# Performance work log

Hardware: AMD Instinct MI355X
Metric: run time of the kernel (lower is better)

Reference implementation:

```python
import jax, jax.numpy as jnp
import numpy as np

INPUT_SIZE = 1024
HIDDEN_SIZE = 1024
B, L = 32, 2048


def setup_inputs() -> dict:
    key = jax.random.key(0)
    k_h, k_m, k_lw, k_vw, k_vq = jax.random.split(key, 5)
    h = jax.random.normal(k_h, (B, L, INPUT_SIZE), dtype=jnp.float32)
    mask = jax.random.randint(k_m, (B, L), 0, 2).astype(bool)
    # nn.Linear(input+hidden, hidden): weight (hidden, input+hidden), bias (hidden,)
    fan = INPUT_SIZE + HIDDEN_SIZE + HIDDEN_SIZE
    ln_w = jax.random.uniform(k_lw, (HIDDEN_SIZE, INPUT_SIZE + HIDDEN_SIZE),
                              minval=-1.0, maxval=1.0, dtype=jnp.float32) * np.sqrt(6.0 / fan)
    ln_b = jnp.zeros((HIDDEN_SIZE,), dtype=jnp.float32)
    # v: Linear(hidden, 1, bias=False) -> weight (1, hidden); store as (hidden,)
    v_w = jax.random.uniform(k_vw, (HIDDEN_SIZE,), minval=-1.0, maxval=1.0,
                             dtype=jnp.float32) * np.sqrt(6.0 / (HIDDEN_SIZE + 1))
    vq = jax.random.uniform(k_vq, (HIDDEN_SIZE,), dtype=jnp.float32)
    return {"h": h, "mask": mask, "ln_w": ln_w, "ln_b": ln_b, "v_w": v_w, "vq": vq}


def reference(h, mask, ln_w, ln_b, v_w, vq):
    # ln(cat([h, vq], -1)) == h @ W_h^T + vq @ W_vq^T + b  (vq is constant over b,l)
    W_h = ln_w[:, :INPUT_SIZE]          # (H, I)
    W_vq = ln_w[:, INPUT_SIZE:]         # (H, H)
    bias = ln_b + W_vq @ vq             # (H,)
    pre = jnp.einsum('bli,hi->blh', h, W_h) + bias  # (B, L, H)
    s = jnp.tanh(pre) @ v_w             # (B, L)
    s = s - (~mask).astype(s.dtype) * 10000.0
    a = jax.nn.softmax(s, axis=1)       # softmax over seq dim
    r = jnp.einsum('bl,bli->bi', a, h)  # (B, I)
    return r  # dropout omitted (eval mode)
```

## Files before the change

kernel.cpp:

```cpp
#include <hip/hip_runtime.h>
#include <hip/hip_bf16.h>

typedef short  bf16x8s __attribute__((ext_vector_type(8)));
typedef float  f32x4   __attribute__((ext_vector_type(4)));

#define BATCH 32
#define SEQL  2048
#define NROWS (BATCH * SEQL)
#define IN    1024
#define HID   1024

#define WHB_OFF   0u
#define BIAS_OFF  0x200000u
#define SPART_OFF 0x210000u
#define ABUF_OFF  0x610000u
#define HB_OFF    0x650000u
#define WS_NEED_BF16 ((size_t)HB_OFF + (size_t)NROWS * IN * 2)

__device__ __forceinline__ unsigned int pack2bf(float f0, float f1) {
    unsigned int u0 = __float_as_uint(f0) + 0x8000u;
    unsigned int u1 = __float_as_uint(f1) + 0x8000u;
    return __builtin_amdgcn_perm(u1, u0, 0x07060302u);
}

__device__ __forceinline__ float tanh_fast(float x) {
    float xc = fminf(fmaxf(x, -15.f), 15.f);
    float t  = __builtin_amdgcn_exp2f(xc * 2.8853900817779268f);
    return (t - 1.f) * __builtin_amdgcn_rcpf(t + 1.f);
}

__device__ __forceinline__ void gl2lds16(const void* g, void* l) {
    __builtin_amdgcn_global_load_lds(
        (const __attribute__((address_space(1))) unsigned int*)g,
        (__attribute__((address_space(3))) unsigned int*)l, 16, 0, 0);
}

__device__ __forceinline__ void block_map(int bi, int& rb, int& cb) {
    int xcd  = bi & 7;
    int slot = bi >> 3;
    rb = xcd + 8 * (slot >> 3);
    cb = slot & 7;
}

__global__ __launch_bounds__(256) void prep_kernel(const float* __restrict__ ln_w,
                                                   const float* __restrict__ ln_b,
                                                   const float* __restrict__ vq,
                                                   const float* __restrict__ h,
                                                   unsigned short* __restrict__ whb,
                                                   float* __restrict__ bias,
                                                   unsigned short* __restrict__ hb) {
    const int bi = blockIdx.x;
    const int t  = threadIdx.x;
    if (bi < 1024) {
        const int n = bi;
        const int wave = t >> 6;
        const int lane = t & 63;
        float4 v = ((const float4*)(ln_w + (size_t)n * 2048))[t];
        uint2 pk;
        pk.x = pack2bf(v.x, v.y);
        pk.y = pack2bf(v.z, v.w);
        *(uint2*)(whb + (size_t)n * 1024 + t * 4) = pk;
        const float* wrow = ln_w + (size_t)n * 2048 + 1024;
        float s = 0.f;
        #pragma unroll
        for (int j = 0; j < 4; ++j) {
            int k = t + j * 256;
            s += wrow[k] * vq[k];
        }
        #pragma unroll
        for (int off = 32; off; off >>= 1) s += __shfl_xor(s, off);
        __shared__ float red[4];
        if (lane == 0) red[wave] = s;
        __syncthreads();
        if (t == 0) bias[n] = ln_b[n] + red[0] + red[1] + red[2] + red[3];
    } else {
        size_t idx = ((size_t)(bi - 1024) * 256 + t) * 8;
        float4 a = *(const float4*)(h + idx);
        float4 b = *(const float4*)(h + idx + 4);
        uint4 p;
        p.x = pack2bf(a.x, a.y); p.y = pack2bf(a.z, a.w);
        p.z = pack2bf(b.x, b.y); p.w = pack2bf(b.z, b.w);
        *(uint4*)(hb + idx) = p;
    }
}

__global__ __launch_bounds__(512) void gemm256_kernel(const unsigned short* __restrict__ hb,
                                                      const unsigned short* __restrict__ whb,
                                                      const float* __restrict__ bias,
                                                      const float* __restrict__ vw,
                                                      float* __restrict__ s_part) {
    __shared__ __align__(16) unsigned short As[8192];
    __shared__ __align__(16) unsigned short Bs[4096];

    const int tid = threadIdx.x;
    int rb, cb;
    block_map(blockIdx.x, rb, cb);
    const int wave = tid >> 6;
    const int lane = tid & 63;
    const int quad = lane >> 4;
    const int l15  = lane & 15;
    const int wy   = wave >> 1;
    const int wx   = wave & 1;
    const int row0 = rb * 256;
    const int col0 = cb * 128;

    const int srow = tid >> 2;
    const int sg   = tid & 3;
    const int swz  = (srow >> 1) & 3;
    const unsigned short* gA0 = hb  + (size_t)(row0 + srow) * 1024 + ((sg ^ swz) * 8);
    const unsigned short* gA1 = gA0 + (size_t)128 * 1024;
    const unsigned short* gB0 = whb + (size_t)(col0 + srow) * 1024 + ((sg ^ swz) * 8);
    unsigned short* lA0 = As + tid * 8;
    unsigned short* lA1 = As + 4096 + tid * 8;
    unsigned short* lB0 = Bs + tid * 8;

    const unsigned short* rA[4];
    const unsigned short* rB[4];
    #pragma unroll
    for (int i = 0; i < 4; ++i) {
        int ra = wy * 64 + i * 16 + l15;
        rA[i] = As + ra * 32 + ((quad ^ ((ra >> 1) & 3)) * 8);
        int rn = wx * 64 + i * 16 + l15;
        rB[i] = Bs + rn * 32 + ((quad ^ ((rn >> 1) & 3)) * 8);
    }

    f32x4 acc[4][4];
    #pragma unroll
    for (int i = 0; i < 4; ++i)
        #pragma unroll
        for (int j = 0; j < 4; ++j)
            acc[i][j] = (f32x4){0.f, 0.f, 0.f, 0.f};

    for (int k0 = 0; k0 < 1024; k0 += 32) {
        __syncthreads();
        gl2lds16(gA0 + k0, lA0);
        gl2lds16(gA1 + k0, lA1);
        gl2lds16(gB0 + k0, lB0);
        __syncthreads();

        bf16x8s af[4], bfv[4];
        #pragma unroll
        for (int i = 0; i < 4; ++i) af[i]  = *(const bf16x8s*)rA[i];
        #pragma unroll
        for (int i = 0; i < 4; ++i) bfv[i] = *(const bf16x8s*)rB[i];
        #pragma unroll
        for (int mt = 0; mt < 4; ++mt)
            #pragma unroll
            for (int nt = 0; nt < 4; ++nt)
                acc[mt][nt] = __builtin_amdgcn_mfma_f32_16x16x32_bf16(af[mt], bfv[nt], acc[mt][nt], 0, 0, 0);
    }

    const int colb = col0 + wx * 64 + l15;
    float vwv[4], bv[4];
    #pragma unroll
    for (int nt = 0; nt < 4; ++nt) {
        vwv[nt] = vw[colb + nt * 16];
        bv[nt]  = bias[colb + nt * 16];
    }
    const int rowb = row0 + wy * 64 + quad * 4;
    float* sp = s_part + (size_t)(cb * 2 + wx) * NROWS;
    #pragma unroll
    for (int mt = 0; mt < 4; ++mt) {
        #pragma unroll
        for (int r = 0; r < 4; ++r) {
            float p = 0.f;
            #pragma unroll
            for (int nt = 0; nt < 4; ++nt)
                p += tanh_fast(acc[mt][nt][r] + bv[nt]) * vwv[nt];
            p += __shfl_xor(p, 1);
            p += __shfl_xor(p, 2);
            p += __shfl_xor(p, 4);
            p += __shfl_xor(p, 8);
            if (l15 == 0) sp[rowb + mt * 16 + r] = p;
        }
    }
}

__global__ __launch_bounds__(256) void gemm_f32_kernel(const float* __restrict__ hmat,
                                                       const unsigned short* __restrict__ whb,
                                                       const float* __restrict__ bias,
                                                       const float* __restrict__ vw,
                                                       float* __restrict__ s_part) {
    __shared__ __align__(16) unsigned short As[4096];
    __shared__ __align__(16) unsigned short Bs[4096];
    const int tid = threadIdx.x;
    int rb, cb;
    block_map(blockIdx.x, rb, cb);
    const int wave = tid >> 6;
    const int lane = tid & 63;
    const int quad = lane >> 4;
    const int l15  = lane & 15;
    const int wy   = wave >> 1;
    const int wx   = wave & 1;
    const int row0 = rb * 128;
    const int col0 = cb * 128;
    const int srow = tid >> 2;
    const int sg   = tid & 3;
    const int swz  = (srow >> 1) & 3;
    const float*          gA0 = hmat + (size_t)(row0 + srow)      * 1024 + sg * 8;
    const float*          gA1 = hmat + (size_t)(row0 + srow + 64) * 1024 + sg * 8;
    const unsigned short* gB0 = whb  + (size_t)(col0 + srow)      * 1024 + ((sg ^ swz) * 8);
    unsigned short* wA0 = As + srow * 32 + ((sg ^ swz) * 8);
    unsigned short* wA1 = wA0 + 64 * 32;
    unsigned short* lB0 = Bs + tid * 8;
    const unsigned short* rA[4];
    const unsigned short* rB[4];
    #pragma unroll
    for (int i = 0; i < 4; ++i) {
        int ra = wy * 64 + i * 16 + l15;
        rA[i] = As + ra * 32 + ((quad ^ ((ra >> 1) & 3)) * 8);
        int rn = wx * 64 + i * 16 + l15;
        rB[i] = Bs + rn * 32 + ((quad ^ ((rn >> 1) & 3)) * 8);
    }
    f32x4 acc[4][4];
    #pragma unroll
    for (int i = 0; i < 4; ++i)
        #pragma unroll
        for (int j = 0; j < 4; ++j)
            acc[i][j] = (f32x4){0.f, 0.f, 0.f, 0.f};
    for (int k0 = 0; k0 < 1024; k0 += 32) {
        float4 va0 = *(const float4*)(gA0 + k0);
        float4 va1 = *(const float4*)(gA0 + k0 + 4);
        float4 va2 = *(const float4*)(gA1 + k0);
        float4 va3 = *(const float4*)(gA1 + k0 + 4);
        __syncthreads();
        gl2lds16(gB0 + k0, lB0);
        gl2lds16(gB0 + 65536 + k0, lB0 + 2048);
        uint4 pa0, pa1;
        pa0.x = pack2bf(va0.x, va0.y); pa0.y = pack2bf(va0.z, va0.w);
        pa0.z = pack2bf(va1.x, va1.y); pa0.w = pack2bf(va1.z, va1.w);
        pa1.x = pack2bf(va2.x, va2.y); pa1.y = pack2bf(va2.z, va2.w);
        pa1.z = pack2bf(va3.x, va3.y); pa1.w = pack2bf(va3.z, va3.w);
        *(uint4*)wA0 = pa0;
        *(uint4*)wA1 = pa1;
        __syncthreads();
        bf16x8s af[4], bfv[4];
        #pragma unroll
        for (int i = 0; i < 4; ++i) af[i]  = *(const bf16x8s*)rA[i];
        #pragma unroll
        for (int i = 0; i < 4; ++i) bfv[i] = *(const bf16x8s*)rB[i];
        #pragma unroll
        for (int mt = 0; mt < 4; ++mt)
            #pragma unroll
            for (int nt = 0; nt < 4; ++nt)
                acc[mt][nt] = __builtin_amdgcn_mfma_f32_16x16x32_bf16(af[mt], bfv[nt], acc[mt][nt], 0, 0, 0);
    }
    const int colb = col0 + wx * 64 + l15;
    float vwv[4], bv[4];
    #pragma unroll
    for (int nt = 0; nt < 4; ++nt) {
        vwv[nt] = vw[colb + nt * 16];
        bv[nt]  = bias[colb + nt * 16];
    }
    const int rowb = row0 + wy * 64 + quad * 4;
    float* sp = s_part + (size_t)(cb * 2 + wx) * NROWS;
    #pragma unroll
    for (int mt = 0; mt < 4; ++mt) {
        #pragma unroll
        for (int r = 0; r < 4; ++r) {
            float p = 0.f;
            #pragma unroll
            for (int nt = 0; nt < 4; ++nt)
                p += tanh_fast(acc[mt][nt][r] + bv[nt]) * vwv[nt];
            p += __shfl_xor(p, 1);
            p += __shfl_xor(p, 2);
            p += __shfl_xor(p, 4);
            p += __shfl_xor(p, 8);
            if (l15 == 0) sp[rowb + mt * 16 + r] = p;
        }
    }
}

__global__ __launch_bounds__(256) void softmax_kernel(const float* __restrict__ s_part,
                                                      const int* __restrict__ mask,
                                                      float* __restrict__ a_buf,
                                                      float* __restrict__ out) {
    const int b    = blockIdx.x;
    const int t    = threadIdx.x;
    const int wave = t >> 6;
    const int lane = t & 63;
    ((float4*)(out + b * 1024))[t] = (float4){0.f, 0.f, 0.f, 0.f};
    __shared__ float redm[4];
    __shared__ float reds[4];
    float sv[8];
    float mx = -3.0e38f;
    #pragma unroll
    for (int j = 0; j < 8; ++j) {
        int l = t + j * 256;
        float v = 0.f;
        #pragma unroll
        for (int c = 0; c < 16; ++c)
            v += s_part[(size_t)c * NROWS + b * 2048 + l];
        if (mask[b * 2048 + l] == 0) v -= 10000.f;
        sv[j] = v;
        mx = fmaxf(mx, v);
    }
    #pragma unroll
    for (int off = 32; off; off >>= 1) mx = fmaxf(mx, __shfl_xor(mx, off));
    if (lane == 0) redm[wave] = mx;
    __syncthreads();
    mx = fmaxf(fmaxf(redm[0], redm[1]), fmaxf(redm[2], redm[3]));
    float sum = 0.f;
    #pragma unroll
    for (int j = 0; j < 8; ++j) {
        sv[j] = __expf(sv[j] - mx);
        sum += sv[j];
    }
    #pragma unroll
    for (int off = 32; off; off >>= 1) sum += __shfl_xor(sum, off);
    if (lane == 0) reds[wave] = sum;
    __syncthreads();
    sum = reds[0] + reds[1] + reds[2] + reds[3];
    float inv = 1.f / sum;
    #pragma unroll
    for (int j = 0; j < 8; ++j)
        a_buf[b * 2048 + t + j * 256] = sv[j] * inv;
}

__global__ __launch_bounds__(256) void r_bf16_kernel(const unsigned short* __restrict__ hb,
                                                     const float* __restrict__ a_buf,
                                                     float* __restrict__ out) {
    const int b  = blockIdx.x >> 5;
    const int lc = blockIdx.x & 31;
    const int t  = threadIdx.x;
    __shared__ float aw[64];
    if (t < 64) aw[t] = a_buf[b * 2048 + lc * 64 + t];
    __syncthreads();
    const uint2* hp = (const uint2*)(hb + (size_t)(b * 2048 + lc * 64) * 1024) + t;
    float a0 = 0.f, a1 = 0.f, a2 = 0.f, a3 = 0.f;
    #pragma unroll 8
    for (int l = 0; l < 64; ++l) {
        uint2 v = hp[(size_t)l * 256];
        float av = aw[l];
        a0 += av * __uint_as_float(v.x << 16);
        a1 += av * __uint_as_float(v.x & 0xffff0000u);
        a2 += av * __uint_as_float(v.y << 16);
        a3 += av * __uint_as_float(v.y & 0xffff0000u);
    }
    float* op = out + b * 1024 + t * 4;
    atomicAdd(op + 0, a0);
    atomicAdd(op + 1, a1);
    atomicAdd(op + 2, a2);
    atomicAdd(op + 3, a3);
}

__global__ __launch_bounds__(256) void r_f32_kernel(const float* __restrict__ hmat,
                                                    const float* __restrict__ a_buf,
                                                    float* __restrict__ out) {
    const int b  = blockIdx.x >> 5;
    const int lc = blockIdx.x & 31;
    const int t  = threadIdx.x;
    __shared__ float aw[64];
    if (t < 64) aw[t] = a_buf[b * 2048 + lc * 64 + t];
    __syncthreads();
    const float4* hp = (const float4*)hmat + (size_t)(b * 2048 + lc * 64) * 256;
    float ax = 0.f, ay = 0.f, az = 0.f, aq = 0.f;
    #pragma unroll 8
    for (int l = 0; l < 64; ++l) {
        float4 hv = hp[(size_t)l * 256 + t];
        float av = aw[l];
        ax += av * hv.x; ay += av * hv.y; az += av * hv.z; aq += av * hv.w;
    }
    float* op = out + b * 1024 + t * 4;
    atomicAdd(op + 0, ax);
    atomicAdd(op + 1, ay);
    atomicAdd(op + 2, az);
    atomicAdd(op + 3, aq);
}

extern "C" void kernel_launch(void* const* d_in, const int* in_sizes, int n_in,
                              void* d_out, int out_size, void* d_ws, size_t ws_size,
                              hipStream_t stream) {
    const float* h    = (const float*)d_in[0];
    const int*   mask = (const int*)d_in[1];
    const float* ln_w = (const float*)d_in[2];
    const float* ln_b = (const float*)d_in[3];
    const float* v_w  = (const float*)d_in[4];
    const float* vq   = (const float*)d_in[5];
    float* out = (float*)d_out;

    char* ws = (char*)d_ws;
    unsigned short* whb = (unsigned short*)(ws + WHB_OFF);
    float* bias         = (float*)(ws + BIAS_OFF);
    float* s_part       = (float*)(ws + SPART_OFF);
    float* a_buf        = (float*)(ws + ABUF_OFF);
    unsigned short* hb  = (unsigned short*)(ws + HB_OFF);

    const bool use_bf16_h = (ws_size >= WS_NEED_BF16);

    if (use_bf16_h) {
        prep_kernel<<<1024 + 32768, 256, 0, stream>>>(ln_w, ln_b, vq, h, whb, bias, hb);
        gemm256_kernel<<<(NROWS / 256) * (HID / 128), 512, 0, stream>>>(hb, whb, bias, v_w, s_part);
        softmax_kernel<<<BATCH, 256, 0, stream>>>(s_part, mask, a_buf, out);
        r_bf16_kernel<<<BATCH * 32, 256, 0, stream>>>(hb, a_buf, out);
    } else {
        prep_kernel<<<1024, 256, 0, stream>>>(ln_w, ln_b, vq, h, whb, bias, hb);
        gemm_f32_kernel<<<(NROWS / 128) * (HID / 128), 256, 0, stream>>>(h, whb, bias, v_w, s_part);
        softmax_kernel<<<BATCH, 256, 0, stream>>>(s_part, mask, a_buf, out);
        r_f32_kernel<<<BATCH * 32, 256, 0, stream>>>(h, a_buf, out);
    }
}
```

Before: 557.7 us.

## Fuse fp32-to-bf16 conversion of h into GEMM A-tile load and transpose s_part

Removes the separate h conversion pass: the GEMM now loads fp32 h rows directly, converts them to bf16 in registers with one-step register prefetch, and writes them into swizzled LDS. The column-block-0 workgroups also store the bf16 copy for the later weighted-sum kernel. The per-column partial scores are stored row-major so softmax can read them with float4 loads, and softmax moves to 512 threads. In exchange, every column block rereads fp32 h (twice the bytes of bf16), and the async global-to-LDS loads for A are replaced by synchronous register loads.

```diff
diff --git a/kernel.cpp b/kernel.cpp
--- a/kernel.cpp
+++ b/kernel.cpp
@@ -45,50 +45,38 @@
 __global__ __launch_bounds__(256) void prep_kernel(const float* __restrict__ ln_w,
                                                    const float* __restrict__ ln_b,
                                                    const float* __restrict__ vq,
-                                                   const float* __restrict__ h,
                                                    unsigned short* __restrict__ whb,
-                                                   float* __restrict__ bias,
-                                                   unsigned short* __restrict__ hb) {
-    const int bi = blockIdx.x;
-    const int t  = threadIdx.x;
-    if (bi < 1024) {
-        const int n = bi;
-        const int wave = t >> 6;
-        const int lane = t & 63;
-        float4 v = ((const float4*)(ln_w + (size_t)n * 2048))[t];
-        uint2 pk;
-        pk.x = pack2bf(v.x, v.y);
-        pk.y = pack2bf(v.z, v.w);
-        *(uint2*)(whb + (size_t)n * 1024 + t * 4) = pk;
-        const float* wrow = ln_w + (size_t)n * 2048 + 1024;
-        float s = 0.f;
-        #pragma unroll
-        for (int j = 0; j < 4; ++j) {
-            int k = t + j * 256;
-            s += wrow[k] * vq[k];
-        }
-        #pragma unroll
-        for (int off = 32; off; off >>= 1) s += __shfl_xor(s, off);
-        __shared__ float red[4];
-        if (lane == 0) red[wave] = s;
-        __syncthreads();
-        if (t == 0) bias[n] = ln_b[n] + red[0] + red[1] + red[2] + red[3];
-    } else {
-        size_t idx = ((size_t)(bi - 1024) * 256 + t) * 8;
-        float4 a = *(const float4*)(h + idx);
-        float4 b = *(const float4*)(h + idx + 4);
-        uint4 p;
-        p.x = pack2bf(a.x, a.y); p.y = pack2bf(a.z, a.w);
-        p.z = pack2bf(b.x, b.y); p.w = pack2bf(b.z, b.w);
-        *(uint4*)(hb + idx) = p;
-    }
-}
-
-__global__ __launch_bounds__(512) void gemm256_kernel(const unsigned short* __restrict__ hb,
-                                                      const unsigned short* __restrict__ whb,
-                                                      const float* __restrict__ bias,
-                                                      const float* __restrict__ vw,
-                                                      float* __restrict__ s_part) {
+                                                   float* __restrict__ bias) {
+    const int n    = blockIdx.x;
+    const int t    = threadIdx.x;
+    const int wave = t >> 6;
+    const int lane = t & 63;
+    float4 v = ((const float4*)(ln_w + (size_t)n * 2048))[t];
+    uint2 pk;
+    pk.x = pack2bf(v.x, v.y);
+    pk.y = pack2bf(v.z, v.w);
+    *(uint2*)(whb + (size_t)n * 1024 + t * 4) = pk;
+    const float* wrow = ln_w + (size_t)n * 2048 + 1024;
+    float s = 0.f;
+    #pragma unroll
+    for (int j = 0; j < 4; ++j) {
+        int k = t + j * 256;
+        s += wrow[k] * vq[k];
+    }
+    #pragma unroll
+    for (int off = 32; off; off >>= 1) s += __shfl_xor(s, off);
+    __shared__ float red[4];
+    if (lane == 0) red[wave] = s;
+    __syncthreads();
+    if (t == 0) bias[n] = ln_b[n] + red[0] + red[1] + red[2] + red[3];
+}
+
+__global__ __launch_bounds__(512) void gemm256_fused_kernel(const float* __restrict__ h,
+                                                            const unsigned short* __restrict__ whb,
+                                                            const float* __restrict__ bias,
+                                                            const float* __restrict__ vw,
+                                                            float* __restrict__ s_part,
+                                                            unsigned short* __restrict__ hb) {
     __shared__ __align__(16) unsigned short As[8192];
     __shared__ __align__(16) unsigned short Bs[4096];
 
@@ -104,14 +92,18 @@
     const int row0 = rb * 256;
     const int col0 = cb * 128;
 
-    const int srow = tid >> 2;
-    const int sg   = tid & 3;
-    const int swz  = (srow >> 1) & 3;
-    const unsigned short* gA0 = hb  + (size_t)(row0 + srow) * 1024 + ((sg ^ swz) * 8);
-    const unsigned short* gA1 = gA0 + (size_t)128 * 1024;
-    const unsigned short* gB0 = whb + (size_t)(col0 + srow) * 1024 + ((sg ^ swz) * 8);
-    unsigned short* lA0 = As + tid * 8;
-    unsigned short* lA1 = As + 4096 + tid * 8;
+    const int srow = tid >> 1;
+    const int half = tid & 1;
+    const int aswz = (srow >> 1) & 3;
+    const float* gA = h + (size_t)(row0 + srow) * 1024 + half * 16;
+    unsigned short* wA0 = As + srow * 32 + (((2 * half)     ^ aswz) * 8);
+    unsigned short* wA1 = As + srow * 32 + (((2 * half + 1) ^ aswz) * 8);
+    unsigned short* hbp = hb + (size_t)(row0 + srow) * 1024 + half * 16;
+
+    const int bsrow = tid >> 2;
+    const int bsg   = tid & 3;
+    const int bswz  = (bsrow >> 1) & 3;
+    const unsigned short* gB0 = whb + (size_t)(col0 + bsrow) * 1024 + ((bsg ^ bswz) * 8);
     unsigned short* lB0 = Bs + tid * 8;
 
     const unsigned short* rA[4];
@@ -131,11 +123,30 @@
         for (int j = 0; j < 4; ++j)
             acc[i][j] = (f32x4){0.f, 0.f, 0.f, 0.f};
 
+    float4 va0 = *(const float4*)(gA);
+    float4 va1 = *(const float4*)(gA + 4);
+    float4 va2 = *(const float4*)(gA + 8);
+    float4 va3 = *(const float4*)(gA + 12);
+
     for (int k0 = 0; k0 < 1024; k0 += 32) {
         __syncthreads();
-        gl2lds16(gA0 + k0, lA0);
-        gl2lds16(gA1 + k0, lA1);
         gl2lds16(gB0 + k0, lB0);
+        uint4 p0, p1;
+        p0.x = pack2bf(va0.x, va0.y); p0.y = pack2bf(va0.z, va0.w);
+        p0.z = pack2bf(va1.x, va1.y); p0.w = pack2bf(va1.z, va1.w);
+        p1.x = pack2bf(va2.x, va2.y); p1.y = pack2bf(va2.z, va2.w);
+        p1.z = pack2bf(va3.x, va3.y); p1.w = pack2bf(va3.z, va3.w);
+        *(uint4*)wA0 = p0;
+        *(uint4*)wA1 = p1;
+        if (cb == 0) {
+            *(uint4*)(hbp + k0)     = p0;
+            *(uint4*)(hbp + k0 + 8) = p1;
+        }
+        const int kn = (k0 + 32) & 1023;
+        va0 = *(const float4*)(gA + kn);
+        va1 = *(const float4*)(gA + kn + 4);
+        va2 = *(const float4*)(gA + kn + 8);
+        va3 = *(const float4*)(gA + kn + 12);
         __syncthreads();
 
         bf16x8s af[4], bfv[4];
@@ -158,7 +169,7 @@
         bv[nt]  = bias[colb + nt * 16];
     }
     const int rowb = row0 + wy * 64 + quad * 4;
-    float* sp = s_part + (size_t)(cb * 2 + wx) * NROWS;
+    const int colp = cb * 2 + wx;
     #pragma unroll
     for (int mt = 0; mt < 4; ++mt) {
         #pragma unroll
@@ -171,7 +182,7 @@
             p += __shfl_xor(p, 2);
             p += __shfl_xor(p, 4);
             p += __shfl_xor(p, 8);
-            if (l15 == 0) sp[rowb + mt * 16 + r] = p;
+            if (l15 == 0) s_part[(size_t)(rowb + mt * 16 + r) * 16 + colp] = p;
         }
     }
 }
@@ -253,7 +264,7 @@
         bv[nt]  = bias[colb + nt * 16];
     }
     const int rowb = row0 + wy * 64 + quad * 4;
-    float* sp = s_part + (size_t)(cb * 2 + wx) * NROWS;
+    const int colp = cb * 2 + wx;
     #pragma unroll
     for (int mt = 0; mt < 4; ++mt) {
         #pragma unroll
@@ -266,12 +277,12 @@
             p += __shfl_xor(p, 2);
             p += __shfl_xor(p, 4);
             p += __shfl_xor(p, 8);
-            if (l15 == 0) sp[rowb + mt * 16 + r] = p;
+            if (l15 == 0) s_part[(size_t)(rowb + mt * 16 + r) * 16 + colp] = p;
         }
     }
 }
 
-__global__ __launch_bounds__(256) void softmax_kernel(const float* __restrict__ s_part,
+__global__ __launch_bounds__(512) void softmax_kernel(const float* __restrict__ s_part,
                                                       const int* __restrict__ mask,
                                                       float* __restrict__ a_buf,
                                                       float* __restrict__ out) {
@@ -279,18 +290,18 @@
     const int t    = threadIdx.x;
     const int wave = t >> 6;
     const int lane = t & 63;
-    ((float4*)(out + b * 1024))[t] = (float4){0.f, 0.f, 0.f, 0.f};
-    __shared__ float redm[4];
-    __shared__ float reds[4];
-    float sv[8];
+    ((float2*)(out + b * 1024))[t] = (float2){0.f, 0.f};
+    __shared__ float redm[8];
+    __shared__ float reds[8];
+    float sv[4];
     float mx = -3.0e38f;
     #pragma unroll
-    for (int j = 0; j < 8; ++j) {
-        int l = t + j * 256;
-        float v = 0.f;
-        #pragma unroll
-        for (int c = 0; c < 16; ++c)
-            v += s_part[(size_t)c * NROWS + b * 2048 + l];
+    for (int j = 0; j < 4; ++j) {
+        int l = t + j * 512;
+        const float4* pr = (const float4*)(s_part + ((size_t)b * 2048 + l) * 16);
+        float4 q0 = pr[0], q1 = pr[1], q2 = pr[2], q3 = pr[3];
+        float v = (q0.x + q0.y + q0.z + q0.w) + (q1.x + q1.y + q1.z + q1.w)
+                + (q2.x + q2.y + q2.z + q2.w) + (q3.x + q3.y + q3.z + q3.w);
         if (mask[b * 2048 + l] == 0) v -= 10000.f;
         sv[j] = v;
         mx = fmaxf(mx, v);
@@ -299,10 +310,12 @@
     for (int off = 32; off; off >>= 1) mx = fmaxf(mx, __shfl_xor(mx, off));
     if (lane == 0) redm[wave] = mx;
     __syncthreads();
-    mx = fmaxf(fmaxf(redm[0], redm[1]), fmaxf(redm[2], redm[3]));
+    mx = redm[0];
+    #pragma unroll
+    for (int w = 1; w < 8; ++w) mx = fmaxf(mx, redm[w]);
     float sum = 0.f;
     #pragma unroll
-    for (int j = 0; j < 8; ++j) {
+    for (int j = 0; j < 4; ++j) {
         sv[j] = __expf(sv[j] - mx);
         sum += sv[j];
     }
@@ -310,11 +323,13 @@
     for (int off = 32; off; off >>= 1) sum += __shfl_xor(sum, off);
     if (lane == 0) reds[wave] = sum;
     __syncthreads();
-    sum = reds[0] + reds[1] + reds[2] + reds[3];
+    sum = reds[0];
+    #pragma unroll
+    for (int w = 1; w < 8; ++w) sum += reds[w];
     float inv = 1.f / sum;
     #pragma unroll
-    for (int j = 0; j < 8; ++j)
-        a_buf[b * 2048 + t + j * 256] = sv[j] * inv;
+    for (int j = 0; j < 4; ++j)
+        a_buf[b * 2048 + t + j * 512] = sv[j] * inv;
 }
 
 __global__ __launch_bounds__(256) void r_bf16_kernel(const unsigned short* __restrict__ hb,
@@ -388,15 +403,14 @@
 
     const bool use_bf16_h = (ws_size >= WS_NEED_BF16);
 
+    prep_kernel<<<1024, 256, 0, stream>>>(ln_w, ln_b, vq, whb, bias);
     if (use_bf16_h) {
-        prep_kernel<<<1024 + 32768, 256, 0, stream>>>(ln_w, ln_b, vq, h, whb, bias, hb);
-        gemm256_kernel<<<(NROWS / 256) * (HID / 128), 512, 0, stream>>>(hb, whb, bias, v_w, s_part);
-        softmax_kernel<<<BATCH, 256, 0, stream>>>(s_part, mask, a_buf, out);
+        gemm256_fused_kernel<<<(NROWS / 256) * (HID / 128), 512, 0, stream>>>(h, whb, bias, v_w, s_part, hb);
+        softmax_kernel<<<BATCH, 512, 0, stream>>>(s_part, mask, a_buf, out);
         r_bf16_kernel<<<BATCH * 32, 256, 0, stream>>>(hb, a_buf, out);
     } else {
-        prep_kernel<<<1024, 256, 0, stream>>>(ln_w, ln_b, vq, h, whb, bias, hb);
         gemm_f32_kernel<<<(NROWS / 128) * (HID / 128), 256, 0, stream>>>(h, whb, bias, v_w, s_part);
-        softmax_kernel<<<BATCH, 256, 0, stream>>>(s_part, mask, a_buf, out);
+        softmax_kernel<<<BATCH, 512, 0, stream>>>(s_part, mask, a_buf, out);
         r_f32_kernel<<<BATCH * 32, 256, 0, stream>>>(h, a_buf, out);
     }
 }
```

New measurement: 595.6 us. +6.8%, slower.

## Double-buffer GEMM LDS tiles and transpose s_part layout for vectorized softmax

Applied to the files above, without the earlier changes.

The bf16 GEMM now keeps two LDS buffers and issues the global-to-LDS loads for the next K tile before computing on the current one, so each iteration needs one barrier instead of two and memory latency can overlap the MFMAs. The partial-score buffer is changed to row-major (16 partials per row), so the softmax kernel reads each row's partials with four float4 loads. The softmax kernel also moves from 256 to 512 threads per block. Doubling LDS raises per-block shared memory, which may reduce occupancy, and the transposed s_part stores from the GEMM epilogue are now strided.

```diff
diff --git a/kernel.cpp b/kernel.cpp
--- a/kernel.cpp
+++ b/kernel.cpp
@@ -89,8 +89,8 @@
                                                       const float* __restrict__ bias,
                                                       const float* __restrict__ vw,
                                                       float* __restrict__ s_part) {
-    __shared__ __align__(16) unsigned short As[8192];
-    __shared__ __align__(16) unsigned short Bs[4096];
+    __shared__ __align__(16) unsigned short As[2][8192];
+    __shared__ __align__(16) unsigned short Bs[2][4096];
 
     const int tid = threadIdx.x;
     int rb, cb;
@@ -110,18 +110,18 @@
     const unsigned short* gA0 = hb  + (size_t)(row0 + srow) * 1024 + ((sg ^ swz) * 8);
     const unsigned short* gA1 = gA0 + (size_t)128 * 1024;
     const unsigned short* gB0 = whb + (size_t)(col0 + srow) * 1024 + ((sg ^ swz) * 8);
-    unsigned short* lA0 = As + tid * 8;
-    unsigned short* lA1 = As + 4096 + tid * 8;
-    unsigned short* lB0 = Bs + tid * 8;
+    const int dA0 = tid * 8;
+    const int dA1 = 4096 + tid * 8;
+    const int dB0 = tid * 8;
 
     const unsigned short* rA[4];
     const unsigned short* rB[4];
     #pragma unroll
     for (int i = 0; i < 4; ++i) {
         int ra = wy * 64 + i * 16 + l15;
-        rA[i] = As + ra * 32 + ((quad ^ ((ra >> 1) & 3)) * 8);
+        rA[i] = &As[0][0] + ra * 32 + ((quad ^ ((ra >> 1) & 3)) * 8);
         int rn = wx * 64 + i * 16 + l15;
-        rB[i] = Bs + rn * 32 + ((quad ^ ((rn >> 1) & 3)) * 8);
+        rB[i] = &Bs[0][0] + rn * 32 + ((quad ^ ((rn >> 1) & 3)) * 8);
     }
 
     f32x4 acc[4][4];
@@ -131,23 +131,35 @@
         for (int j = 0; j < 4; ++j)
             acc[i][j] = (f32x4){0.f, 0.f, 0.f, 0.f};
 
+    gl2lds16(gA0, &As[0][dA0]);
+    gl2lds16(gA1, &As[0][dA1]);
+    gl2lds16(gB0, &Bs[0][dB0]);
+    __syncthreads();
+
+    int cur = 0;
     for (int k0 = 0; k0 < 1024; k0 += 32) {
-        __syncthreads();
-        gl2lds16(gA0 + k0, lA0);
-        gl2lds16(gA1 + k0, lA1);
-        gl2lds16(gB0 + k0, lB0);
-        __syncthreads();
-
+        if (k0 + 32 < 1024) {
+            const int nxt = cur ^ 1;
+            gl2lds16(gA0 + k0 + 32, &As[nxt][dA0]);
+            gl2lds16(gA1 + k0 + 32, &As[nxt][dA1]);
+            gl2lds16(gB0 + k0 + 32, &Bs[nxt][dB0]);
+        }
+
+        const int aoff = cur * 8192;
+        const int boff = cur * 4096;
         bf16x8s af[4], bfv[4];
         #pragma unroll
-        for (int i = 0; i < 4; ++i) af[i]  = *(const bf16x8s*)rA[i];
-        #pragma unroll
-        for (int i = 0; i < 4; ++i) bfv[i] = *(const bf16x8s*)rB[i];
+        for (int i = 0; i < 4; ++i) af[i]  = *(const bf16x8s*)(rA[i] + aoff);
+        #pragma unroll
+        for (int i = 0; i < 4; ++i) bfv[i] = *(const bf16x8s*)(rB[i] + boff);
         #pragma unroll
         for (int mt = 0; mt < 4; ++mt)
             #pragma unroll
             for (int nt = 0; nt < 4; ++nt)
                 acc[mt][nt] = __builtin_amdgcn_mfma_f32_16x16x32_bf16(af[mt], bfv[nt], acc[mt][nt], 0, 0, 0);
+
+        __syncthreads();
+        cur ^= 1;
     }
 
     const int colb = col0 + wx * 64 + l15;
@@ -158,7 +170,7 @@
         bv[nt]  = bias[colb + nt * 16];
     }
     const int rowb = row0 + wy * 64 + quad * 4;
-    float* sp = s_part + (size_t)(cb * 2 + wx) * NROWS;
+    const int colp = cb * 2 + wx;
     #pragma unroll
     for (int mt = 0; mt < 4; ++mt) {
         #pragma unroll
@@ -171,7 +183,7 @@
             p += __shfl_xor(p, 2);
             p += __shfl_xor(p, 4);
             p += __shfl_xor(p, 8);
-            if (l15 == 0) sp[rowb + mt * 16 + r] = p;
+            if (l15 == 0) s_part[(size_t)(rowb + mt * 16 + r) * 16 + colp] = p;
         }
     }
 }
@@ -253,7 +265,7 @@
         bv[nt]  = bias[colb + nt * 16];
     }
     const int rowb = row0 + wy * 64 + quad * 4;
-    float* sp = s_part + (size_t)(cb * 2 + wx) * NROWS;
+    const int colp = cb * 2 + wx;
     #pragma unroll
     for (int mt = 0; mt < 4; ++mt) {
         #pragma unroll
@@ -266,12 +278,12 @@
             p += __shfl_xor(p, 2);
             p += __shfl_xor(p, 4);
             p += __shfl_xor(p, 8);
-            if (l15 == 0) sp[rowb + mt * 16 + r] = p;
+            if (l15 == 0) s_part[(size_t)(rowb + mt * 16 + r) * 16 + colp] = p;
         }
     }
 }
 
-__global__ __launch_bounds__(256) void softmax_kernel(const float* __restrict__ s_part,
+__global__ __launch_bounds__(512) void softmax_kernel(const float* __restrict__ s_part,
                                                       const int* __restrict__ mask,
                                                       float* __restrict__ a_buf,
                                                       float* __restrict__ out) {
@@ -279,18 +291,18 @@
     const int t    = threadIdx.x;
     const int wave = t >> 6;
     const int lane = t & 63;
-    ((float4*)(out + b * 1024))[t] = (float4){0.f, 0.f, 0.f, 0.f};
-    __shared__ float redm[4];
-    __shared__ float reds[4];
-    float sv[8];
+    ((float2*)(out + b * 1024))[t] = (float2){0.f, 0.f};
+    __shared__ float redm[8];
+    __shared__ float reds[8];
+    float sv[4];
     float mx = -3.0e38f;
     #pragma unroll
-    for (int j = 0; j < 8; ++j) {
-        int l = t + j * 256;
-        float v = 0.f;
-        #pragma unroll
-        for (int c = 0; c < 16; ++c)
-            v += s_part[(size_t)c * NROWS + b * 2048 + l];
+    for (int j = 0; j < 4; ++j) {
+        int l = t + j * 512;
+        const float4* pr = (const float4*)(s_part + ((size_t)b * 2048 + l) * 16);
+        float4 q0 = pr[0], q1 = pr[1], q2 = pr[2], q3 = pr[3];
+        float v = (q0.x + q0.y + q0.z + q0.w) + (q1.x + q1.y + q1.z + q1.w)
+                + (q2.x + q2.y + q2.z + q2.w) + (q3.x + q3.y + q3.z + q3.w);
         if (mask[b * 2048 + l] == 0) v -= 10000.f;
         sv[j] = v;
         mx = fmaxf(mx, v);
@@ -299,10 +311,12 @@
     for (int off = 32; off; off >>= 1) mx = fmaxf(mx, __shfl_xor(mx, off));
     if (lane == 0) redm[wave] = mx;
     __syncthreads();
-    mx = fmaxf(fmaxf(redm[0], redm[1]), fmaxf(redm[2], redm[3]));
+    mx = redm[0];
+    #pragma unroll
+    for (int w = 1; w < 8; ++w) mx = fmaxf(mx, redm[w]);
     float sum = 0.f;
     #pragma unroll
-    for (int j = 0; j < 8; ++j) {
+    for (int j = 0; j < 4; ++j) {
         sv[j] = __expf(sv[j] - mx);
         sum += sv[j];
     }
@@ -310,11 +324,13 @@
     for (int off = 32; off; off >>= 1) sum += __shfl_xor(sum, off);
     if (lane == 0) reds[wave] = sum;
     __syncthreads();
-    sum = reds[0] + reds[1] + reds[2] + reds[3];
+    sum = reds[0];
+    #pragma unroll
+    for (int w = 1; w < 8; ++w) sum += reds[w];
     float inv = 1.f / sum;
     #pragma unroll
-    for (int j = 0; j < 8; ++j)
-        a_buf[b * 2048 + t + j * 256] = sv[j] * inv;
+    for (int j = 0; j < 4; ++j)
+        a_buf[b * 2048 + t + j * 512] = sv[j] * inv;
 }
 
 __global__ __launch_bounds__(256) void r_bf16_kernel(const unsigned short* __restrict__ hb,
@@ -391,12 +407,12 @@
     if (use_bf16_h) {
         prep_kernel<<<1024 + 32768, 256, 0, stream>>>(ln_w, ln_b, vq, h, whb, bias, hb);
         gemm256_kernel<<<(NROWS / 256) * (HID / 128), 512, 0, stream>>>(hb, whb, bias, v_w, s_part);
-        softmax_kernel<<<BATCH, 256, 0, stream>>>(s_part, mask, a_buf, out);
+        softmax_kernel<<<BATCH, 512, 0, stream>>>(s_part, mask, a_buf, out);
         r_bf16_kernel<<<BATCH * 32, 256, 0, stream>>>(hb, a_buf, out);
     } else {
         prep_kernel<<<1024, 256, 0, stream>>>(ln_w, ln_b, vq, h, whb, bias, hb);
         gemm_f32_kernel<<<(NROWS / 128) * (HID / 128), 256, 0, stream>>>(h, whb, bias, v_w, s_part);
-        softmax_kernel<<<BATCH, 256, 0, stream>>>(s_part, mask, a_buf, out);
+        softmax_kernel<<<BATCH, 512, 0, stream>>>(s_part, mask, a_buf, out);
         r_f32_kernel<<<BATCH * 32, 256, 0, stream>>>(h, a_buf, out);
     }
 }
```

Result: slower. 643.2 us (+15.3%).
